# Kernel tuning notes

Hardware: AMD Instinct MI355X
Metric: run time of the kernel (lower is better)

## Reference

```python
import jax, jax.numpy as jnp
import numpy as np

EPS = 1e-5
B, N = 16, 131072

def _bn(x, g, b, m, v):
    # x: [C, N]; inference-mode batchnorm with given stats
    return g[:, None] * (x - m[:, None]) * jax.lax.rsqrt(v[:, None] + EPS) + b[:, None]

def _make_npts():
    base = N // B
    offs = np.linspace(-2048, 2048, B).astype(np.int64)
    npts = np.full(B, base, dtype=np.int64) + offs
    npts[-1] += N - npts.sum()
    assert npts.sum() == N and (npts > 0).all()
    return npts

def setup_inputs() -> dict:
    key = jax.random.key(0)
    ks = jax.random.split(key, 16)
    d = {}
    d["x"] = jax.random.normal(ks[0], (3, N), jnp.float32)
    d["npts"] = jnp.asarray(_make_npts(), jnp.int32)
    def w(k, o, i):
        return jax.random.normal(k, (o, i), jnp.float32) * (1.0 / np.sqrt(i))
    def bnp(k, c):
        k1, k2, k3, k4 = jax.random.split(k, 4)
        return (1.0 + 0.1 * jax.random.normal(k1, (c,), jnp.float32),
                0.1 * jax.random.normal(k2, (c,), jnp.float32),
                0.1 * jax.random.normal(k3, (c,), jnp.float32),
                0.5 + jax.random.uniform(k4, (c,), jnp.float32))
    d["W1"] = w(ks[1], 128, 3);   d["b1"] = jnp.zeros(128, jnp.float32)
    d["g1"], d["be1"], d["m1"], d["v1"] = bnp(ks[2], 128)
    d["W2"] = w(ks[3], 256, 128); d["b2"] = jnp.zeros(256, jnp.float32)
    d["g2"], d["be2"], d["m2"], d["v2"] = bnp(ks[4], 256)
    d["W3"] = w(ks[5], 512, 512); d["b3"] = jnp.zeros(512, jnp.float32)
    d["g3"], d["be3"], d["m3"], d["v3"] = bnp(ks[6], 512)
    d["W4"] = w(ks[7], 1024, 512); d["b4"] = jnp.zeros(1024, jnp.float32)
    d["g4"], d["be4"], d["m4"], d["v4"] = bnp(ks[8], 1024)
    return d

def reference(x, npts,
              W1, b1, g1, be1, m1, v1,
              W2, b2, g2, be2, m2, v2,
              W3, b3, g3, be3, m3, v3,
              W4, b4, g4, be4, m4, v4):
    # segment ids for the ragged point->cloud mapping (replaces torch.split loops)
    seg = jnp.repeat(jnp.arange(B, dtype=jnp.int32), npts, total_repeat_length=N)  # [N]
    h = jax.nn.relu(_bn(W1 @ x + b1[:, None], g1, be1, m1, v1))        # [128, N]
    f = _bn(W2 @ h + b2[:, None], g2, be2, m2, v2)                      # [256, N]
    g = jax.ops.segment_max(f.T, seg, num_segments=B)                   # [B, 256]
    gs = g[seg].T                                                       # [256, N] broadcast back
    xc = jnp.concatenate([gs, f], axis=0)                               # [512, N]
    h3 = jax.nn.relu(_bn(W3 @ xc + b3[:, None], g3, be3, m3, v3))       # [512, N]
    h4 = _bn(W4 @ h3 + b4[:, None], g4, be4, m4, v4)                    # [1024, N]
    v = jax.ops.segment_max(h4.T, seg, num_segments=B)                  # [B, 1024]
    return v
```

## Files before the change

### kernel.cpp

```cpp
#include <hip/hip_runtime.h>
#include <hip/hip_bf16.h>
#include <stdint.h>

#define NTOT 131072
#define NSEG 16
#define EPSV 1e-5f

typedef __attribute__((ext_vector_type(8))) short bf16x8;
typedef __attribute__((ext_vector_type(4))) float f32x4;

struct Args {
  const float* x; const int* npts;
  const float *W1,*b1,*g1,*be1,*m1,*v1;
  const float *W2,*b2,*g2,*be2,*m2,*v2;
  const float *W3,*b3,*g3,*be3,*m3,*v3;
  const float *W4,*b4,*g4,*be4,*m4,*v4;
  int* offs;
  float *a1,*c1,*a2,*c2,*a3,*c3,*a4,*c4;
  unsigned int *gkeys,*vkeys;
  unsigned short *w2b;
  unsigned short *w3p;
  unsigned short *w4p;
  unsigned short *fbufp;
  unsigned short *h3p;
  float* cseg;
  float* out;
};

__device__ inline unsigned int f2key(float f){ unsigned u=__float_as_uint(f); return (u&0x80000000u)? ~u : (u|0x80000000u); }
__device__ inline float key2f(unsigned k){ unsigned u=(k&0x80000000u)? (k^0x80000000u) : ~k; return __uint_as_float(u); }
__device__ inline unsigned short f2bf(float f){ __hip_bfloat16 h=__float2bfloat16(f); return *(unsigned short*)&h; }

__device__ inline void gl16(const void* g, void* l){
  __builtin_amdgcn_global_load_lds((const __attribute__((address_space(1))) unsigned int*)g,
                                   (__attribute__((address_space(3))) unsigned int*)l, 16, 0, 0);
}

__global__ void k_setup(Args A){
  int tid = threadIdx.x;
  if (tid==0){ int s=0; A.offs[0]=0; for (int i=0;i<NSEG;i++){ s+=A.npts[i]; A.offs[i+1]=s; } }
  for (int c=tid;c<128;c+=256){ float a=A.g1[c]*rsqrtf(A.v1[c]+EPSV); A.a1[c]=a; A.c1[c]=A.be1[c]+a*(A.b1[c]-A.m1[c]); }
  for (int c=tid;c<256;c+=256){ float a=A.g2[c]*rsqrtf(A.v2[c]+EPSV); A.a2[c]=a; A.c2[c]=A.be2[c]+a*(A.b2[c]-A.m2[c]); }
  for (int c=tid;c<512;c+=256){ float a=A.g3[c]*rsqrtf(A.v3[c]+EPSV); A.a3[c]=a; A.c3[c]=A.be3[c]+a*(A.b3[c]-A.m3[c]); }
  for (int c=tid;c<1024;c+=256){ float a=A.g4[c]*rsqrtf(A.v4[c]+EPSV); A.a4[c]=a; A.c4[c]=A.be4[c]+a*(A.b4[c]-A.m4[c]); }
  for (int i=tid;i<NSEG*256;i+=256)  A.gkeys[i]=0u;
  for (int i=tid;i<NSEG*1024;i+=256) A.vkeys[i]=0u;
}

__global__ void k_conv(Args A){
  const int n1=256*128;
  const int n2=131072;
  const int n3=524288;
  for (int i = blockIdx.x*256+threadIdx.x; i < n1+n2+n3; i += gridDim.x*256){
    if (i<n1) A.w2b[i]=f2bf(A.W2[i]);
    else if (i<n1+n2){
      int o=i-n1; int j=o&7, cout=(o>>3)&255, kgrel=(o>>11)&3, ks=(o>>13)&7, cg=(o>>16)&1;
      A.w3p[o]=f2bf(A.W3[(size_t)(cg*256+cout)*512 + 256 + ks*32 + kgrel*8 + j]);
    } else {
      int o=i-n1-n2; int j=o&7, cout=(o>>3)&255, kgrel=(o>>11)&3, ks=(o>>13)&15, cg=(o>>17)&3;
      A.w4p[o]=f2bf(A.W4[(size_t)(cg*256+cout)*512 + ks*32 + kgrel*8 + j]);
    }
  }
}

__global__ __launch_bounds__(256) void k_l12(Args A){
  __shared__ float w1s[384], a1s[128], c1s[128], a2s[256], c2s[256];
  __shared__ float xs[3][64];
  __shared__ int offs_s[NSEG+1], segp[64];
  __shared__ unsigned short hs[16*64*8];
  int tid=threadIdx.x, pt0=blockIdx.x*64;
  for (int i=tid;i<384;i+=256) w1s[i]=A.W1[i];
  if (tid<128){ a1s[tid]=A.a1[tid]; c1s[tid]=A.c1[tid]; }
  a2s[tid]=A.a2[tid]; c2s[tid]=A.c2[tid];
  if (tid<=NSEG) offs_s[tid]=A.offs[tid];
  if (tid<64){ xs[0][tid]=A.x[pt0+tid]; xs[1][tid]=A.x[NTOT+pt0+tid]; xs[2][tid]=A.x[2*NTOT+pt0+tid]; }
  __syncthreads();
  if (tid<64){ int gp=pt0+tid, s=0; while (gp>=offs_s[s+1]) s++; segp[tid]=s; }
  for (int pair=tid; pair<1024; pair+=256){
    int pt=pair&63, kc=pair>>6;
    float x0=xs[0][pt], x1=xs[1][pt], x2=xs[2][pt];
    unsigned short us[8];
    #pragma unroll
    for (int j=0;j<8;j++){
      int cin=kc*8+j;
      float v = fmaf(w1s[cin*3],x0, fmaf(w1s[cin*3+1],x1, w1s[cin*3+2]*x2));
      v = fmaxf(fmaf(a1s[cin],v,c1s[cin]), 0.f);
      us[j]=f2bf(v);
    }
    uint4 pk;
    pk.x=(unsigned)us[0]|((unsigned)us[1]<<16); pk.y=(unsigned)us[2]|((unsigned)us[3]<<16);
    pk.z=(unsigned)us[4]|((unsigned)us[5]<<16); pk.w=(unsigned)us[6]|((unsigned)us[7]<<16);
    *(uint4*)(&hs[(kc*64+pt)*8]) = pk;
  }
  __syncthreads();
  int lane=tid&63, wv=tid>>6, quad=lane>>4, l16=lane&15;
  int m0=wv*64;
  f32x4 acc[4][4];
  for (int a=0;a<4;a++)
    for (int b=0;b<4;b++)
      acc[a][b]=(f32x4){0.f,0.f,0.f,0.f};
  #pragma unroll
  for (int ks=0; ks<4; ++ks){
    bf16x8 bfr[4];
    #pragma unroll
    for (int nt=0; nt<4; ++nt) bfr[nt]=*(bf16x8*)(&hs[((ks*4+quad)*64 + nt*16 + l16)*8]);
    #pragma unroll
    for (int mt=0; mt<4; ++mt){
      bf16x8 afr = *(const bf16x8*)(&A.w2b[(m0+mt*16+l16)*128 + ks*32 + quad*8]);
      #pragma unroll
      for (int nt=0; nt<4; ++nt)
        acc[mt][nt]=__builtin_amdgcn_mfma_f32_16x16x32_bf16(afr, bfr[nt], acc[mt][nt], 0,0,0);
    }
  }
  bool uni = (segp[0]==segp[63]); int seg0=segp[0];
  size_t tb = (size_t)(blockIdx.x>>2)*65536;
  int prelb = (blockIdx.x&3)*64;
  #pragma unroll
  for (int mt=0;mt<4;++mt){
    int cout0=m0+mt*16+quad*4;
    int kg=cout0>>3, sub=cout0&7;
    float fv[4][4];
    #pragma unroll
    for (int nt=0;nt<4;++nt)
      #pragma unroll
      for (int r=0;r<4;++r)
        fv[nt][r]=fmaf(a2s[cout0+r], acc[mt][nt][r], c2s[cout0+r]);
    #pragma unroll
    for (int nt=0;nt<4;++nt){
      int ptl=nt*16+l16;
      uint2 pk;
      pk.x=(unsigned)f2bf(fv[nt][0])|((unsigned)f2bf(fv[nt][1])<<16);
      pk.y=(unsigned)f2bf(fv[nt][2])|((unsigned)f2bf(fv[nt][3])<<16);
      *(uint2*)&A.fbufp[tb + (size_t)((kg*256 + prelb + ptl)*8 + sub)] = pk;
    }
    #pragma unroll
    for (int r=0;r<4;++r){
      if (uni){
        float mv=fmaxf(fmaxf(fv[0][r],fv[1][r]),fmaxf(fv[2][r],fv[3][r]));
        #pragma unroll
        for (int off=8;off>=1;off>>=1) mv=fmaxf(mv, __shfl_xor(mv,off));
        if (l16==0) atomicMax(&A.gkeys[seg0*256+cout0+r], f2key(mv));
      } else {
        #pragma unroll
        for (int nt=0;nt<4;++nt)
          atomicMax(&A.gkeys[segp[nt*16+l16]*256+cout0+r], f2key(fv[nt][r]));
      }
    }
  }
}

__global__ void k_cseg(Args A){
  int seg = blockIdx.x>>1; int cout = (blockIdx.x&1)*256 + threadIdx.x;
  __shared__ float gs[256];
  gs[threadIdx.x] = key2f(A.gkeys[seg*256+threadIdx.x]);
  __syncthreads();
  const float* wrow = A.W3 + (size_t)cout*512;
  float s=0.f;
  #pragma unroll 8
  for (int k=0;k<256;k++) s = fmaf(wrow[k], gs[k], s);
  A.cseg[seg*512+cout]=s;
}

__global__ __launch_bounds__(512,2) void k_l3(Args A){
  __shared__ unsigned short sA[4][8192];
  __shared__ unsigned short sB[4][8192];
  __shared__ int offs_s[NSEG+1];
  const int NS=8;
  int bid=blockIdx.x, xcd=bid&7, j=bid>>3;
  int cgrp=j&1, ptblk=xcd*64+(j>>1);
  int tid=threadIdx.x, lane=tid&63, wv=tid>>6, quad=lane>>4, l16=lane&15;
  int mq=wv&1, tq=wv>>1;
  const char* wbase0 = (const char*)A.w3p + (size_t)cgrp*131072;
  const char* bbase0 = (const char*)A.fbufp + (size_t)ptblk*131072;
  if (tid<=NSEG) offs_s[tid]=A.offs[tid];

  auto stage=[&](int buf, int s){
    char* lA=(char*)&sA[buf][0];
    char* lB=(char*)&sB[buf][0];
    if (wv<4){
      const char* src = wbase0 + (size_t)s*16384;
      #pragma unroll
      for (int i=0;i<4;++i){ int c=wv*4+i; gl16(src + c*1024 + lane*16, lA + c*1024); }
    } else {
      const char* src = bbase0 + (size_t)s*16384;
      #pragma unroll
      for (int i=0;i<4;++i){ int c=(wv-4)*4+i; gl16(src + c*1024 + lane*16, lB + c*1024); }
    }
  };

  f32x4 acc[8][4];
  for (int a=0;a<8;a++)
    for (int b=0;b<4;b++)
      acc[a][b]=(f32x4){0.f,0.f,0.f,0.f};

  stage(0,0); stage(1,1);
  asm volatile("s_waitcnt lgkmcnt(0)" ::: "memory");
  asm volatile("s_waitcnt vmcnt(4)" ::: "memory");
  __builtin_amdgcn_s_barrier();
  __builtin_amdgcn_sched_barrier(0);

  #pragma unroll
  for (int s=0;s<NS;++s){
    int cur=s&3;
    if (s+2<NS) stage((s+2)&3, s+2);
    if (s+2<NS)      asm volatile("s_waitcnt vmcnt(8)" ::: "memory");
    else if (s+1<NS) asm volatile("s_waitcnt vmcnt(4)" ::: "memory");
    else             asm volatile("s_waitcnt vmcnt(0)" ::: "memory");
    __builtin_amdgcn_s_barrier();
    __builtin_amdgcn_sched_barrier(0);
    bf16x8 afr[8], bb[4];
    #pragma unroll
    for (int mt=0;mt<8;++mt) afr[mt]=*(const bf16x8*)(&sA[cur][(quad*256 + mq*128 + mt*16 + l16)*8]);
    #pragma unroll
    for (int nt=0;nt<4;++nt) bb[nt]=*(const bf16x8*)(&sB[cur][(quad*256 + tq*64 + nt*16 + l16)*8]);
    __builtin_amdgcn_s_setprio(1);
    #pragma unroll
    for (int mt=0;mt<8;++mt)
      #pragma unroll
      for (int nt=0;nt<4;++nt)
        acc[mt][nt]=__builtin_amdgcn_mfma_f32_16x16x32_bf16(afr[mt], bb[nt], acc[mt][nt], 0,0,0);
    __builtin_amdgcn_s_setprio(0);
  }

  int pt0 = ptblk*256 + tq*64;
  int sBeg=0; while (pt0 >= offs_s[sBeg+1]) sBeg++;
  int sEnd=sBeg; while (pt0+63 >= offs_s[sEnd+1]) sEnd++;
  bool uni=(sBeg==sEnd);
  int segl[4];
  if (!uni){
    #pragma unroll
    for (int nt=0;nt<4;++nt){ int gp=pt0+nt*16+l16, ss=sBeg; while (gp>=offs_s[ss+1]) ss++; segl[nt]=ss; }
  }
  size_t hb = (size_t)ptblk*131072;
  #pragma unroll
  for (int mt=0;mt<8;++mt){
    int cout0=cgrp*256 + mq*128 + mt*16 + quad*4;
    int kg=cout0>>3, sub=cout0&7;
    float sa[4],sc[4],csr[4];
    #pragma unroll
    for (int r=0;r<4;++r){ sa[r]=A.a3[cout0+r]; sc[r]=A.c3[cout0+r]; }
    if (uni){
      #pragma unroll
      for (int r=0;r<4;++r) csr[r]=A.cseg[sBeg*512+cout0+r];
    }
    #pragma unroll
    for (int nt=0;nt<4;++nt){
      int prel=tq*64+nt*16+l16;
      unsigned short us[4];
      #pragma unroll
      for (int r=0;r<4;++r){
        float cv = uni? csr[r] : A.cseg[segl[nt]*512+cout0+r];
        float hv = fmaxf(fmaf(sa[r], acc[mt][nt][r]+cv, sc[r]), 0.f);
        us[r]=f2bf(hv);
      }
      uint2 pk;
      pk.x=(unsigned)us[0]|((unsigned)us[1]<<16);
      pk.y=(unsigned)us[2]|((unsigned)us[3]<<16);
      *(uint2*)&A.h3p[hb + (size_t)((kg*256+prel)*8+sub)] = pk;
    }
  }
}

__global__ __launch_bounds__(512,2) void k_l4(Args A){
  __shared__ unsigned short sA[4][8192];
  __shared__ unsigned short sB[4][8192];
  __shared__ int offs_s[NSEG+1];
  const int NS=16;
  int bid=blockIdx.x, xcd=bid&7, j=bid>>3;
  int cgrp=j&3, ptblk=xcd*64+(j>>2);
  int tid=threadIdx.x, lane=tid&63, wv=tid>>6, quad=lane>>4, l16=lane&15;
  int mq=wv&1, tq=wv>>1;
  const char* wbase0 = (const char*)A.w4p + (size_t)cgrp*262144;
  const char* bbase0 = (const char*)A.h3p + (size_t)ptblk*262144;
  if (tid<=NSEG) offs_s[tid]=A.offs[tid];

  auto stage=[&](int buf, int s){
    char* lA=(char*)&sA[buf][0];
    char* lB=(char*)&sB[buf][0];
    if (wv<4){
      const char* src = wbase0 + (size_t)s*16384;
      #pragma unroll
      for (int i=0;i<4;++i){ int c=wv*4+i; gl16(src + c*1024 + lane*16, lA + c*1024); }
    } else {
      const char* src = bbase0 + (size_t)s*16384;
      #pragma unroll
      for (int i=0;i<4;++i){ int c=(wv-4)*4+i; gl16(src + c*1024 + lane*16, lB + c*1024); }
    }
  };

  f32x4 acc[8][4];
  for (int a=0;a<8;a++)
    for (int b=0;b<4;b++)
      acc[a][b]=(f32x4){0.f,0.f,0.f,0.f};

  stage(0,0); stage(1,1);
  asm volatile("s_waitcnt lgkmcnt(0)" ::: "memory");
  asm volatile("s_waitcnt vmcnt(4)" ::: "memory");
  __builtin_amdgcn_s_barrier();
  __builtin_amdgcn_sched_barrier(0);

  #pragma unroll
  for (int s=0;s<NS;++s){
    int cur=s&3;
    if (s+2<NS) stage((s+2)&3, s+2);
    if (s+2<NS)      asm volatile("s_waitcnt vmcnt(8)" ::: "memory");
    else if (s+1<NS) asm volatile("s_waitcnt vmcnt(4)" ::: "memory");
    else             asm volatile("s_waitcnt vmcnt(0)" ::: "memory");
    __builtin_amdgcn_s_barrier();
    __builtin_amdgcn_sched_barrier(0);
    bf16x8 afr[8], bb[4];
    #pragma unroll
    for (int mt=0;mt<8;++mt) afr[mt]=*(const bf16x8*)(&sA[cur][(quad*256 + mq*128 + mt*16 + l16)*8]);
    #pragma unroll
    for (int nt=0;nt<4;++nt) bb[nt]=*(const bf16x8*)(&sB[cur][(quad*256 + tq*64 + nt*16 + l16)*8]);
    __builtin_amdgcn_s_setprio(1);
    #pragma unroll
    for (int mt=0;mt<8;++mt)
      #pragma unroll
      for (int nt=0;nt<4;++nt)
        acc[mt][nt]=__builtin_amdgcn_mfma_f32_16x16x32_bf16(afr[mt], bb[nt], acc[mt][nt], 0,0,0);
    __builtin_amdgcn_s_setprio(0);
  }

  int pt0 = ptblk*256 + tq*64;
  int sBeg=0; while (pt0 >= offs_s[sBeg+1]) sBeg++;
  int sEnd=sBeg; while (pt0+63 >= offs_s[sEnd+1]) sEnd++;
  bool uni=(sBeg==sEnd);
  int segl[4];
  if (!uni){
    #pragma unroll
    for (int nt=0;nt<4;++nt){ int gp=pt0+nt*16+l16, ss=sBeg; while (gp>=offs_s[ss+1]) ss++; segl[nt]=ss; }
  }
  #pragma unroll
  for (int mt=0;mt<8;++mt){
    int cout0=cgrp*256 + mq*128 + mt*16 + quad*4;
    #pragma unroll
    for (int r=0;r<4;++r){
      int cout=cout0+r;
      float sa=A.a4[cout], sc=A.c4[cout];
      float mv=-3.4e38f;
      #pragma unroll
      for (int nt=0;nt<4;++nt){
        float fv=fmaf(sa, acc[mt][nt][r], sc);
        if (uni) mv=fmaxf(mv,fv);
        else atomicMax(&A.vkeys[segl[nt]*1024+cout], f2key(fv));
      }
      if (uni){
        #pragma unroll
        for (int off=8;off>=1;off>>=1) mv=fmaxf(mv, __shfl_xor(mv,off));
        if (l16==0) atomicMax(&A.vkeys[sBeg*1024+cout], f2key(mv));
      }
    }
  }
}

__global__ void k_final(Args A){
  int i=blockIdx.x*256+threadIdx.x;
  if (i<NSEG*1024) A.out[i]=key2f(A.vkeys[i]);
}

extern "C" void kernel_launch(void* const* d_in, const int* in_sizes, int n_in,
                              void* d_out, int out_size, void* d_ws, size_t ws_size,
                              hipStream_t stream){
  Args A;
  A.x  =(const float*)d_in[0];  A.npts=(const int*)d_in[1];
  A.W1 =(const float*)d_in[2];  A.b1 =(const float*)d_in[3];
  A.g1 =(const float*)d_in[4];  A.be1=(const float*)d_in[5];
  A.m1 =(const float*)d_in[6];  A.v1 =(const float*)d_in[7];
  A.W2 =(const float*)d_in[8];  A.b2 =(const float*)d_in[9];
  A.g2 =(const float*)d_in[10]; A.be2=(const float*)d_in[11];
  A.m2 =(const float*)d_in[12]; A.v2 =(const float*)d_in[13];
  A.W3 =(const float*)d_in[14]; A.b3 =(const float*)d_in[15];
  A.g3 =(const float*)d_in[16]; A.be3=(const float*)d_in[17];
  A.m3 =(const float*)d_in[18]; A.v3 =(const float*)d_in[19];
  A.W4 =(const float*)d_in[20]; A.b4 =(const float*)d_in[21];
  A.g4 =(const float*)d_in[22]; A.be4=(const float*)d_in[23];
  A.m4 =(const float*)d_in[24]; A.v4 =(const float*)d_in[25];

  char* w=(char*)d_ws;
  auto alloc=[&](size_t b)->void*{ void* p=(void*)w; w += (b+255)&~(size_t)255; return p; };
  A.offs =(int*)alloc((NSEG+1)*4);
  A.a1=(float*)alloc(128*4);  A.c1=(float*)alloc(128*4);
  A.a2=(float*)alloc(256*4);  A.c2=(float*)alloc(256*4);
  A.a3=(float*)alloc(512*4);  A.c3=(float*)alloc(512*4);
  A.a4=(float*)alloc(1024*4); A.c4=(float*)alloc(1024*4);
  A.gkeys=(unsigned int*)alloc(NSEG*256*4);
  A.vkeys=(unsigned int*)alloc(NSEG*1024*4);
  A.cseg =(float*)alloc(NSEG*512*4);
  A.w2b=(unsigned short*)alloc(256*128*2);
  A.w3p=(unsigned short*)alloc(131072*2);
  A.w4p=(unsigned short*)alloc(524288*2);
  A.fbufp=(unsigned short*)alloc((size_t)512*65536*2);
  A.h3p  =(unsigned short*)alloc((size_t)512*131072*2);
  A.out=(float*)d_out;

  k_setup<<<dim3(1),dim3(256),0,stream>>>(A);
  k_conv <<<dim3(2688),dim3(256),0,stream>>>(A);
  k_l12  <<<dim3(NTOT/64),dim3(256),0,stream>>>(A);
  k_cseg <<<dim3(32),dim3(256),0,stream>>>(A);
  k_l3   <<<dim3(1024),dim3(512),0,stream>>>(A);
  k_l4   <<<dim3(2048),dim3(512),0,stream>>>(A);
  k_final<<<dim3(64),dim3(256),0,stream>>>(A);
}
```

Before: 728.3 us.

## Restructure L3/L4 GEMM pipeline with 64-deep K tiles and split A/B staging

Rewrites the main loops of the layer-3 and layer-4 bf16 MFMA GEMMs to use double-buffered 64-wide K tiles instead of four-deep 32-wide buffers. The A and B copies are interleaved into the MFMA phases: next-tile weights are issued early and B is prefetched two tiles ahead, with barriers placed mid-iteration. The wave layout changes to 2x4 (wm/wn), and launch bounds drop to one block per SM. The aim is fewer barriers per unit of work and better overlap of global-to-LDS copies with MFMA, at the cost of lower occupancy and a more delicate vmcnt/barrier protocol.

```diff
diff --git a/kernel.cpp b/kernel.cpp
--- a/kernel.cpp
+++ b/kernel.cpp
@@ -161,31 +161,29 @@
   A.cseg[seg*512+cout]=s;
 }
 
-__global__ __launch_bounds__(512,2) void k_l3(Args A){
-  __shared__ unsigned short sA[4][8192];
-  __shared__ unsigned short sB[4][8192];
+__global__ __launch_bounds__(512,1) void k_l3(Args A){
+  __shared__ unsigned short sA[2][16384], sB[2][16384];
   __shared__ int offs_s[NSEG+1];
-  const int NS=8;
-  int bid=blockIdx.x, xcd=bid&7, j=bid>>3;
-  int cgrp=j&1, ptblk=xcd*64+(j>>1);
+  const int NT=4;
+  int bid=blockIdx.x, xcd=bid&7, idx=bid>>3;
+  int Mt=idx&1, ptblk=xcd*64+(idx>>1);
   int tid=threadIdx.x, lane=tid&63, wv=tid>>6, quad=lane>>4, l16=lane&15;
-  int mq=wv&1, tq=wv>>1;
-  const char* wbase0 = (const char*)A.w3p + (size_t)cgrp*131072;
-  const char* bbase0 = (const char*)A.fbufp + (size_t)ptblk*131072;
+  int wm=wv>>2, wn=wv&3;
+  const char* wsrc=(const char*)A.w3p   + (size_t)Mt*131072;
+  const char* bsrc=(const char*)A.fbufp + (size_t)ptblk*131072;
   if (tid<=NSEG) offs_s[tid]=A.offs[tid];
 
-  auto stage=[&](int buf, int s){
-    char* lA=(char*)&sA[buf][0];
-    char* lB=(char*)&sB[buf][0];
-    if (wv<4){
-      const char* src = wbase0 + (size_t)s*16384;
-      #pragma unroll
-      for (int i=0;i<4;++i){ int c=wv*4+i; gl16(src + c*1024 + lane*16, lA + c*1024); }
-    } else {
-      const char* src = bbase0 + (size_t)s*16384;
-      #pragma unroll
-      for (int i=0;i<4;++i){ int c=(wv-4)*4+i; gl16(src + c*1024 + lane*16, lB + c*1024); }
-    }
+  auto stageA=[&](int kt,int h){
+    const char* s = wsrc + kt*32768 + h*16384;
+    char* d = (char*)&sA[kt&1][0] + h*16384;
+    gl16(s + wv*1024 + lane*16, d + wv*1024);
+    gl16(s + 8192 + wv*1024 + lane*16, d + 8192 + wv*1024);
+  };
+  auto stageB=[&](int kt,int h){
+    const char* s = bsrc + kt*32768 + h*16384;
+    char* d = (char*)&sB[kt&1][0] + h*16384;
+    gl16(s + wv*1024 + lane*16, d + wv*1024);
+    gl16(s + 8192 + wv*1024 + lane*16, d + 8192 + wv*1024);
   };
 
   f32x4 acc[8][4];
@@ -193,36 +191,52 @@
     for (int b=0;b<4;b++)
       acc[a][b]=(f32x4){0.f,0.f,0.f,0.f};
 
-  stage(0,0); stage(1,1);
-  asm volatile("s_waitcnt lgkmcnt(0)" ::: "memory");
+  stageB(0,0); stageB(0,1); stageA(0,0); stageA(0,1); stageB(1,0); stageB(1,1);
   asm volatile("s_waitcnt vmcnt(4)" ::: "memory");
   __builtin_amdgcn_s_barrier();
   __builtin_amdgcn_sched_barrier(0);
 
   #pragma unroll
-  for (int s=0;s<NS;++s){
-    int cur=s&3;
-    if (s+2<NS) stage((s+2)&3, s+2);
-    if (s+2<NS)      asm volatile("s_waitcnt vmcnt(8)" ::: "memory");
-    else if (s+1<NS) asm volatile("s_waitcnt vmcnt(4)" ::: "memory");
-    else             asm volatile("s_waitcnt vmcnt(0)" ::: "memory");
-    __builtin_amdgcn_s_barrier();
-    __builtin_amdgcn_sched_barrier(0);
-    bf16x8 afr[8], bb[4];
-    #pragma unroll
-    for (int mt=0;mt<8;++mt) afr[mt]=*(const bf16x8*)(&sA[cur][(quad*256 + mq*128 + mt*16 + l16)*8]);
-    #pragma unroll
-    for (int nt=0;nt<4;++nt) bb[nt]=*(const bf16x8*)(&sB[cur][(quad*256 + tq*64 + nt*16 + l16)*8]);
-    __builtin_amdgcn_s_setprio(1);
-    #pragma unroll
-    for (int mt=0;mt<8;++mt)
+  for (int kt=0; kt<NT; ++kt){
+    const int P=kt&1;
+    bf16x8 bfr[2][4];
+    #pragma unroll
+    for (int ks=0;ks<2;++ks)
       #pragma unroll
       for (int nt=0;nt<4;++nt)
-        acc[mt][nt]=__builtin_amdgcn_mfma_f32_16x16x32_bf16(afr[mt], bb[nt], acc[mt][nt], 0,0,0);
-    __builtin_amdgcn_s_setprio(0);
-  }
-
-  int pt0 = ptblk*256 + tq*64;
+        bfr[ks][nt]=*(const bf16x8*)(&sB[P][((ks*4+quad)*256 + wn*64 + nt*16 + l16)*8]);
+    #pragma unroll
+    for (int p=0;p<4;++p){
+      bf16x8 afr[2][2];
+      #pragma unroll
+      for (int ks=0;ks<2;++ks)
+        #pragma unroll
+        for (int mi=0;mi<2;++mi)
+          afr[ks][mi]=*(const bf16x8*)(&sA[P][((ks*4+quad)*256 + wm*128 + (p*2+mi)*16 + l16)*8]);
+      if (p==0 && kt+1<NT) stageA(kt+1,0);
+      if (p==1 && kt+1<NT) stageA(kt+1,1);
+      if (p==2 && kt+2<NT) stageB(kt+2,0);
+      if (p==3 && kt+2<NT) stageB(kt+2,1);
+      __builtin_amdgcn_s_setprio(1);
+      #pragma unroll
+      for (int ks=0;ks<2;++ks)
+        #pragma unroll
+        for (int mi=0;mi<2;++mi)
+          #pragma unroll
+          for (int nt=0;nt<4;++nt)
+            acc[p*2+mi][nt]=__builtin_amdgcn_mfma_f32_16x16x32_bf16(afr[ks][mi], bfr[ks][nt], acc[p*2+mi][nt],0,0,0);
+      __builtin_amdgcn_s_setprio(0);
+      if (p==1) __builtin_amdgcn_s_barrier();
+      if (p==3){
+        if (kt+2<NT) asm volatile("s_waitcnt vmcnt(4)" ::: "memory");
+        else         asm volatile("s_waitcnt vmcnt(0)" ::: "memory");
+        if (kt+1<NT) __builtin_amdgcn_s_barrier();
+        __builtin_amdgcn_sched_barrier(0);
+      }
+    }
+  }
+
+  int pt0 = ptblk*256 + wn*64;
   int sBeg=0; while (pt0 >= offs_s[sBeg+1]) sBeg++;
   int sEnd=sBeg; while (pt0+63 >= offs_s[sEnd+1]) sEnd++;
   bool uni=(sBeg==sEnd);
@@ -234,7 +248,7 @@
   size_t hb = (size_t)ptblk*131072;
   #pragma unroll
   for (int mt=0;mt<8;++mt){
-    int cout0=cgrp*256 + mq*128 + mt*16 + quad*4;
+    int cout0=Mt*256 + wm*128 + mt*16 + quad*4;
     int kg=cout0>>3, sub=cout0&7;
     float sa[4],sc[4],csr[4];
     #pragma unroll
@@ -245,7 +259,7 @@
     }
     #pragma unroll
     for (int nt=0;nt<4;++nt){
-      int prel=tq*64+nt*16+l16;
+      int prel=wn*64+nt*16+l16;
       unsigned short us[4];
       #pragma unroll
       for (int r=0;r<4;++r){
@@ -261,31 +275,29 @@
   }
 }
 
-__global__ __launch_bounds__(512,2) void k_l4(Args A){
-  __shared__ unsigned short sA[4][8192];
-  __shared__ unsigned short sB[4][8192];
+__global__ __launch_bounds__(512,1) void k_l4(Args A){
+  __shared__ unsigned short sA[2][16384], sB[2][16384];
   __shared__ int offs_s[NSEG+1];
-  const int NS=16;
-  int bid=blockIdx.x, xcd=bid&7, j=bid>>3;
-  int cgrp=j&3, ptblk=xcd*64+(j>>2);
+  const int NT=8;
+  int bid=blockIdx.x, xcd=bid&7, idx=bid>>3;
+  int Mt=idx&3, ptblk=xcd*64+(idx>>2);
   int tid=threadIdx.x, lane=tid&63, wv=tid>>6, quad=lane>>4, l16=lane&15;
-  int mq=wv&1, tq=wv>>1;
-  const char* wbase0 = (const char*)A.w4p + (size_t)cgrp*262144;
-  const char* bbase0 = (const char*)A.h3p + (size_t)ptblk*262144;
+  int wm=wv>>2, wn=wv&3;
+  const char* wsrc=(const char*)A.w4p + (size_t)Mt*262144;
+  const char* bsrc=(const char*)A.h3p + (size_t)ptblk*262144;
   if (tid<=NSEG) offs_s[tid]=A.offs[tid];
 
-  auto stage=[&](int buf, int s){
-    char* lA=(char*)&sA[buf][0];
-    char* lB=(char*)&sB[buf][0];
-    if (wv<4){
-      const char* src = wbase0 + (size_t)s*16384;
-      #pragma unroll
-      for (int i=0;i<4;++i){ int c=wv*4+i; gl16(src + c*1024 + lane*16, lA + c*1024); }
-    } else {
-      const char* src = bbase0 + (size_t)s*16384;
-      #pragma unroll
-      for (int i=0;i<4;++i){ int c=(wv-4)*4+i; gl16(src + c*1024 + lane*16, lB + c*1024); }
-    }
+  auto stageA=[&](int kt,int h){
+    const char* s = wsrc + kt*32768 + h*16384;
+    char* d = (char*)&sA[kt&1][0] + h*16384;
+    gl16(s + wv*1024 + lane*16, d + wv*1024);
+    gl16(s + 8192 + wv*1024 + lane*16, d + 8192 + wv*1024);
+  };
+  auto stageB=[&](int kt,int h){
+    const char* s = bsrc + kt*32768 + h*16384;
+    char* d = (char*)&sB[kt&1][0] + h*16384;
+    gl16(s + wv*1024 + lane*16, d + wv*1024);
+    gl16(s + 8192 + wv*1024 + lane*16, d + 8192 + wv*1024);
   };
 
   f32x4 acc[8][4];
@@ -293,36 +305,52 @@
     for (int b=0;b<4;b++)
       acc[a][b]=(f32x4){0.f,0.f,0.f,0.f};
 
-  stage(0,0); stage(1,1);
-  asm volatile("s_waitcnt lgkmcnt(0)" ::: "memory");
+  stageB(0,0); stageB(0,1); stageA(0,0); stageA(0,1); stageB(1,0); stageB(1,1);
   asm volatile("s_waitcnt vmcnt(4)" ::: "memory");
   __builtin_amdgcn_s_barrier();
   __builtin_amdgcn_sched_barrier(0);
 
   #pragma unroll
-  for (int s=0;s<NS;++s){
-    int cur=s&3;
-    if (s+2<NS) stage((s+2)&3, s+2);
-    if (s+2<NS)      asm volatile("s_waitcnt vmcnt(8)" ::: "memory");
-    else if (s+1<NS) asm volatile("s_waitcnt vmcnt(4)" ::: "memory");
-    else             asm volatile("s_waitcnt vmcnt(0)" ::: "memory");
-    __builtin_amdgcn_s_barrier();
-    __builtin_amdgcn_sched_barrier(0);
-    bf16x8 afr[8], bb[4];
-    #pragma unroll
-    for (int mt=0;mt<8;++mt) afr[mt]=*(const bf16x8*)(&sA[cur][(quad*256 + mq*128 + mt*16 + l16)*8]);
-    #pragma unroll
-    for (int nt=0;nt<4;++nt) bb[nt]=*(const bf16x8*)(&sB[cur][(quad*256 + tq*64 + nt*16 + l16)*8]);
-    __builtin_amdgcn_s_setprio(1);
-    #pragma unroll
-    for (int mt=0;mt<8;++mt)
+  for (int kt=0; kt<NT; ++kt){
+    const int P=kt&1;
+    bf16x8 bfr[2][4];
+    #pragma unroll
+    for (int ks=0;ks<2;++ks)
       #pragma unroll
       for (int nt=0;nt<4;++nt)
-        acc[mt][nt]=__builtin_amdgcn_mfma_f32_16x16x32_bf16(afr[mt], bb[nt], acc[mt][nt], 0,0,0);
-    __builtin_amdgcn_s_setprio(0);
-  }
-
-  int pt0 = ptblk*256 + tq*64;
+        bfr[ks][nt]=*(const bf16x8*)(&sB[P][((ks*4+quad)*256 + wn*64 + nt*16 + l16)*8]);
+    #pragma unroll
+    for (int p=0;p<4;++p){
+      bf16x8 afr[2][2];
+      #pragma unroll
+      for (int ks=0;ks<2;++ks)
+        #pragma unroll
+        for (int mi=0;mi<2;++mi)
+          afr[ks][mi]=*(const bf16x8*)(&sA[P][((ks*4+quad)*256 + wm*128 + (p*2+mi)*16 + l16)*8]);
+      if (p==0 && kt+1<NT) stageA(kt+1,0);
+      if (p==1 && kt+1<NT) stageA(kt+1,1);
+      if (p==2 && kt+2<NT) stageB(kt+2,0);
+      if (p==3 && kt+2<NT) stageB(kt+2,1);
+      __builtin_amdgcn_s_setprio(1);
+      #pragma unroll
+      for (int ks=0;ks<2;++ks)
+        #pragma unroll
+        for (int mi=0;mi<2;++mi)
+          #pragma unroll
+          for (int nt=0;nt<4;++nt)
+            acc[p*2+mi][nt]=__builtin_amdgcn_mfma_f32_16x16x32_bf16(afr[ks][mi], bfr[ks][nt], acc[p*2+mi][nt],0,0,0);
+      __builtin_amdgcn_s_setprio(0);
+      if (p==1) __builtin_amdgcn_s_barrier();
+      if (p==3){
+        if (kt+2<NT) asm volatile("s_waitcnt vmcnt(4)" ::: "memory");
+        else         asm volatile("s_waitcnt vmcnt(0)" ::: "memory");
+        if (kt+1<NT) __builtin_amdgcn_s_barrier();
+        __builtin_amdgcn_sched_barrier(0);
+      }
+    }
+  }
+
+  int pt0 = ptblk*256 + wn*64;
   int sBeg=0; while (pt0 >= offs_s[sBeg+1]) sBeg++;
   int sEnd=sBeg; while (pt0+63 >= offs_s[sEnd+1]) sEnd++;
   bool uni=(sBeg==sEnd);
@@ -333,7 +361,7 @@
   }
   #pragma unroll
   for (int mt=0;mt<8;++mt){
-    int cout0=cgrp*256 + mq*128 + mt*16 + quad*4;
+    int cout0=Mt*256 + wm*128 + mt*16 + quad*4;
     #pragma unroll
     for (int r=0;r<4;++r){
       int cout=cout0+r;
```

Result: slower. 750.7 us (+3.1%).
